# Kernel tuning notes

Hardware: AMD Instinct MI355X
Metric: run time of the kernel (lower is better)

The kernel has to match this reference:

```python
import jax, jax.numpy as jnp
import numpy as np

N_NODES = 50000
N_EDGES = 800000
N_GRAPHS = 64
IN_CH = 128
HID = [64, 128]
MLP_CH = [128, 64, 64, 64, 1]


def _glorot(key, fan_in, fan_out):
    lim = jnp.sqrt(6.0 / (fan_in + fan_out))
    return jax.random.uniform(key, (fan_in, fan_out), jnp.float32, -lim, lim)


def setup_inputs() -> dict:
    key = jax.random.key(0)
    ks = jax.random.split(key, 16)
    x = jax.random.normal(ks[0], (N_NODES, IN_CH), jnp.float32)
    edge_index = jax.random.randint(ks[1], (2, N_EDGES), 0, N_NODES, jnp.int64)
    batch = jnp.sort(jax.random.randint(ks[2], (N_NODES,), 0, N_GRAPHS, jnp.int64))
    inp = {"x": x, "edge_index": edge_index, "batch": batch}
    # GCNConv weights (x @ W + b)
    inp["W1"] = _glorot(ks[3], IN_CH, HID[0]);  inp["b1"] = jnp.zeros((HID[0],), jnp.float32)
    inp["W2"] = _glorot(ks[4], HID[0], HID[1]); inp["b2"] = jnp.zeros((HID[1],), jnp.float32)
    # MLP weights
    for i in range(4):
        inp[f"M{i+1}"] = _glorot(ks[5 + i], MLP_CH[i], MLP_CH[i + 1])
        inp[f"c{i+1}"] = jnp.zeros((MLP_CH[i + 1],), jnp.float32)
    return inp


def _gcn_conv(x, src, dst, dinv, W, b):
    # x' = D^-1/2 (A + I) D^-1/2 (x W) + b, via gather-scale-scatter over edges
    h = x @ W                                   # [N, F]
    norm = dinv[src] * dinv[dst]                # [E+N]
    msg = h[src] * norm[:, None]                # gather + scale
    out = jax.ops.segment_sum(msg, dst, num_segments=x.shape[0])
    return out + b


def reference(x, edge_index, batch, W1, b1, W2, b2, M1, c1, M2, c2, M3, c3, M4, c4):
    N = x.shape[0]
    x = x.astype(jnp.float32)
    # add self loops (PyG GCNConv default)
    loops = jnp.arange(N, dtype=edge_index.dtype)
    src = jnp.concatenate([edge_index[0], loops])
    dst = jnp.concatenate([edge_index[1], loops])
    deg = jax.ops.segment_sum(jnp.ones_like(src, jnp.float32), dst, num_segments=N)
    dinv = jnp.where(deg > 0, jax.lax.rsqrt(jnp.maximum(deg, 1.0)), 0.0)

    h = jax.nn.relu(_gcn_conv(x, src, dst, dinv, W1, b1))
    h = jax.nn.relu(_gcn_conv(h, src, dst, dinv, W2, b2))

    # global mean pool per graph
    sums = jax.ops.segment_sum(h, batch, num_segments=N_GRAPHS)
    cnts = jax.ops.segment_sum(jnp.ones((N,), jnp.float32), batch, num_segments=N_GRAPHS)
    g = sums / jnp.maximum(cnts, 1.0)[:, None]   # [G, 128]

    # MLP (eval mode: dropout is identity)
    g = jax.nn.leaky_relu(g @ M1 + c1, negative_slope=0.2)
    g = jax.nn.leaky_relu(g @ M2 + c2, negative_slope=0.1)
    g = jax.nn.leaky_relu(g @ M3 + c3, negative_slope=0.1)
    g = jax.nn.relu(g @ M4 + c4)
    return g
```

## Files before the change

### kernel.cpp

```cpp
#include <hip/hip_runtime.h>
#include <hip/hip_fp16.h>

#define N_NODES 50000
#define N_EDGES 800000
#define N_GRAPHS 64

#define SCAN_BLOCK 256
#define SCAN_ITEMS 4
#define SCAN_CHUNK (SCAN_BLOCK * SCAN_ITEMS)
#define NB_SCAN ((N_NODES + SCAN_CHUNK - 1) / SCAN_CHUNK)

#define FILL_STRIPES 256

struct __align__(8) h4v { __half2 a, b; };


__global__ void k_zero(int* __restrict__ deg, float* __restrict__ sums) {
    int i = blockIdx.x * 256 + threadIdx.x;
    if (i < N_NODES) deg[i] = 0;
    if (i < N_GRAPHS * 128) sums[i] = 0.f;
}


__global__ void k_deg_part(const int* __restrict__ dst, int* __restrict__ deg, int E) {
    const int range = blockIdx.x & 7;
    const int stripe = blockIdx.x >> 3;
    const int lo = range * (N_NODES / 8);
    const int hi = lo + (N_NODES / 8);
    for (int e = stripe * 256 + threadIdx.x; e < E; e += FILL_STRIPES * 256) {
        int d = dst[e];
        if (d >= lo && d < hi) atomicAdd(&deg[d], 1);
    }
}

__global__ void k_scan1(const int* __restrict__ deg, int* __restrict__ part) {
    __shared__ int lds[SCAN_BLOCK];
    int b = blockIdx.x, t = threadIdx.x;
    int base = b * SCAN_CHUNK + t * SCAN_ITEMS;
    int s = 0;
#pragma unroll
    for (int k = 0; k < SCAN_ITEMS; ++k) {
        int i = base + k;
        if (i < N_NODES) s += deg[i];
    }
    lds[t] = s;
    __syncthreads();
    for (int off = SCAN_BLOCK / 2; off > 0; off >>= 1) {
        if (t < off) lds[t] += lds[t + off];
        __syncthreads();
    }
    if (t == 0) part[b] = lds[0];
}

__global__ void k_scan3(const int* __restrict__ deg, const int* __restrict__ part,
                        int* __restrict__ row_ptr, int* __restrict__ fill,
                        float* __restrict__ dinv) {
    __shared__ int lds[SCAN_BLOCK];
    __shared__ int pl[64];
    __shared__ int basePfx;
    int b = blockIdx.x, t = threadIdx.x;
    if (t < NB_SCAN) pl[t] = part[t];
    int base = b * SCAN_CHUNK + t * SCAN_ITEMS;
    int v[SCAN_ITEMS];
    int s = 0;
#pragma unroll
    for (int k = 0; k < SCAN_ITEMS; ++k) {
        int i = base + k;
        v[k] = (i < N_NODES) ? deg[i] : 0;
        s += v[k];
    }
    lds[t] = s;
    __syncthreads();
    if (t == 0) {
        int acc = 0;
        for (int i = 0; i < b; ++i) acc += pl[i];
        basePfx = acc;
    }
    for (int off = 1; off < SCAN_BLOCK; off <<= 1) {
        int val = (t >= off) ? lds[t - off] : 0;
        __syncthreads();
        lds[t] += val;
        __syncthreads();
    }
    int excl = (t == 0 ? 0 : lds[t - 1]) + basePfx;
#pragma unroll
    for (int k = 0; k < SCAN_ITEMS; ++k) {
        int i = base + k;
        if (i < N_NODES) {
            row_ptr[i] = excl;
            fill[i] = excl;
            dinv[i] = rsqrtf((float)(v[k] + 1));
            excl += v[k];
            if (i == N_NODES - 1) row_ptr[N_NODES] = excl;
        }
    }
}

__global__ void k_fill_part(const int* __restrict__ src, const int* __restrict__ dst,
                            int* __restrict__ fill, unsigned short* __restrict__ csr, int E) {
    const int range = blockIdx.x & 7;
    const int stripe = blockIdx.x >> 3;
    const int lo = range * (N_NODES / 8);
    const int hi = lo + (N_NODES / 8);
    for (int e = stripe * 256 + threadIdx.x; e < E; e += FILL_STRIPES * 256) {
        int d = dst[e];
        if (d >= lo && d < hi) {
            int pos = atomicAdd(&fill[d], 1);
            csr[pos] = (unsigned short)src[e];
        }
    }
}


__global__ __launch_bounds__(256) void k_gemm1(const float* __restrict__ A,
                                               const float* __restrict__ W,
                                               const float* __restrict__ dscale,
                                               __half* __restrict__ Cout, int N) {
    const int FIN = 128;
    __shared__ __align__(16) float As[64 * (FIN + 2)];
    __shared__ __align__(16) float Wsm[FIN * 64];
    const int t = threadIdx.x;
    const int row0 = blockIdx.x * 64;

    const int NF4 = 64 * FIN / 4;
    for (int idx = t; idx < NF4; idx += 256) {
        int r = idx / (FIN / 4);
        int c4 = idx % (FIN / 4);
        float4 v = make_float4(0.f, 0.f, 0.f, 0.f);
        if (row0 + r < N) v = ((const float4*)(A + (size_t)(row0 + r) * FIN))[c4];
        float* p = &As[r * (FIN + 2) + c4 * 4];
        ((float2*)p)[0] = make_float2(v.x, v.y);
        ((float2*)p)[1] = make_float2(v.z, v.w);
    }
    for (int idx = t; idx < FIN * 16; idx += 256) {
        int r = idx / 16, c4 = idx % 16;
        *((float4*)&Wsm[r * 64 + c4 * 4]) = ((const float4*)(W + (size_t)r * 64))[c4];
    }
    __syncthreads();

    const int tc = (t & 15) * 4;
    const int tr = (t >> 4) * 4;
    float acc[4][4] = {};
#pragma unroll 4
    for (int k = 0; k < FIN; k += 2) {
        float2 a[4];
#pragma unroll
        for (int r = 0; r < 4; ++r)
            a[r] = *(const float2*)&As[(tr + r) * (FIN + 2) + k];
        float4 w0 = *(const float4*)&Wsm[k * 64 + tc];
        float4 w1 = *(const float4*)&Wsm[(k + 1) * 64 + tc];
#pragma unroll
        for (int r = 0; r < 4; ++r) {
            acc[r][0] = fmaf(a[r].x, w0.x, acc[r][0]);
            acc[r][1] = fmaf(a[r].x, w0.y, acc[r][1]);
            acc[r][2] = fmaf(a[r].x, w0.z, acc[r][2]);
            acc[r][3] = fmaf(a[r].x, w0.w, acc[r][3]);
            acc[r][0] = fmaf(a[r].y, w1.x, acc[r][0]);
            acc[r][1] = fmaf(a[r].y, w1.y, acc[r][1]);
            acc[r][2] = fmaf(a[r].y, w1.z, acc[r][2]);
            acc[r][3] = fmaf(a[r].y, w1.w, acc[r][3]);
        }
    }

#pragma unroll
    for (int r = 0; r < 4; ++r) {
        int row = row0 + tr + r;
        if (row < N) {
            float s = dscale[row];
            __half2* dsth = (__half2*)(Cout + (size_t)row * 64 + tc);
            dsth[0] = __floats2half2_rn(acc[r][0] * s, acc[r][1] * s);
            dsth[1] = __floats2half2_rn(acc[r][2] * s, acc[r][3] * s);
        }
    }
}


template <bool RELU>
__global__ void k_agg(const h4v* __restrict__ h, const float* __restrict__ dinv,
                      const int* __restrict__ row_ptr, const unsigned short* __restrict__ csr,
                      const float* __restrict__ bias, h4v* __restrict__ out, int N) {
    int node = blockIdx.x * 16 + (threadIdx.x >> 4);
    int lane = threadIdx.x & 15;
    if (node >= N) return;
    float di = dinv[node];
    h4v sv = h[(size_t)node * 16 + lane];
    float2 pa = __half22float2(sv.a), pb = __half22float2(sv.b);
    float x0 = pa.x, y0 = pa.y, z0 = pb.x, w0 = pb.y;
    float x1 = 0, y1 = 0, z1 = 0, w1 = 0;
    float x2 = 0, y2 = 0, z2 = 0, w2 = 0;
    float x3 = 0, y3 = 0, z3 = 0, w3 = 0;
    int beg = row_ptr[node], end = row_ptr[node + 1];
    int j = beg;
    for (; j + 4 <= end; j += 4) {
        int s0 = csr[j], s1 = csr[j + 1], s2 = csr[j + 2], s3 = csr[j + 3];
        h4v v0 = h[(size_t)s0 * 16 + lane];
        h4v v1 = h[(size_t)s1 * 16 + lane];
        h4v v2 = h[(size_t)s2 * 16 + lane];
        h4v v3 = h[(size_t)s3 * 16 + lane];
        float2 a0 = __half22float2(v0.a), b0 = __half22float2(v0.b);
        float2 a1 = __half22float2(v1.a), b1 = __half22float2(v1.b);
        float2 a2 = __half22float2(v2.a), b2 = __half22float2(v2.b);
        float2 a3 = __half22float2(v3.a), b3 = __half22float2(v3.b);
        x0 += a0.x; y0 += a0.y; z0 += b0.x; w0 += b0.y;
        x1 += a1.x; y1 += a1.y; z1 += b1.x; w1 += b1.y;
        x2 += a2.x; y2 += a2.y; z2 += b2.x; w2 += b2.y;
        x3 += a3.x; y3 += a3.y; z3 += b3.x; w3 += b3.y;
    }
    for (; j < end; ++j) {
        h4v v = h[(size_t)csr[j] * 16 + lane];
        float2 a = __half22float2(v.a), b = __half22float2(v.b);
        x0 += a.x; y0 += a.y; z0 += b.x; w0 += b.y;
    }
    float sx = (x0 + x1) + (x2 + x3);
    float sy = (y0 + y1) + (y2 + y3);
    float sz = (z0 + z1) + (z2 + z3);
    float sw = (w0 + w1) + (w2 + w3);
    h4v o;
    if (RELU) {
        float4 bv = ((const float4*)bias)[lane];
        float vx = fmaf(sx, di, bv.x); vx = vx > 0.f ? vx : 0.f;
        float vy = fmaf(sy, di, bv.y); vy = vy > 0.f ? vy : 0.f;
        float vz = fmaf(sz, di, bv.z); vz = vz > 0.f ? vz : 0.f;
        float vw = fmaf(sw, di, bv.w); vw = vw > 0.f ? vw : 0.f;
        o.a = __floats2half2_rn(di * vx, di * vy);
        o.b = __floats2half2_rn(di * vz, di * vw);
    } else {
        o.a = __floats2half2_rn(sx * di, sy * di);
        o.b = __floats2half2_rn(sz * di, sw * di);
    }
    out[(size_t)node * 16 + lane] = o;
}


__global__ __launch_bounds__(256) void k_gemm_pool(const __half2* __restrict__ A2,
                                                   const float* __restrict__ W,
                                                   const float* __restrict__ bias,
                                                   const int* __restrict__ batch,
                                                   float* __restrict__ sums, int N) {
    __shared__ __align__(16) float As[64 * 66];
    __shared__ __align__(16) float Wsm[64 * 64];
    __shared__ float red[16][68];
    __shared__ int batchLDS[64];
    const int t = threadIdx.x;
    const int row0 = blockIdx.x * 64;
    const int coff = blockIdx.y * 64;

    for (int idx = t; idx < 64 * 32; idx += 256) {
        int r = idx >> 5, c2 = idx & 31;
        float2 v = make_float2(0.f, 0.f);
        if (row0 + r < N) v = __half22float2(A2[(size_t)(row0 + r) * 32 + c2]);
        *(float2*)&As[r * 66 + c2 * 2] = v;
    }
    for (int idx = t; idx < 64 * 16; idx += 256) {
        int r = idx >> 4, c4 = idx & 15;
        *(float4*)&Wsm[r * 64 + c4 * 4] = *(const float4*)&W[(size_t)r * 128 + coff + c4 * 4];
    }
    if (t < 64) batchLDS[t] = batch[min(row0 + t, N - 1)];
    __syncthreads();

    const int tc = (t & 15) * 4;
    const int tr = (t >> 4) * 4;
    float acc[4][4] = {};
#pragma unroll 4
    for (int k = 0; k < 64; k += 2) {
        float2 a[4];
#pragma unroll
        for (int r = 0; r < 4; ++r)
            a[r] = *(const float2*)&As[(tr + r) * 66 + k];
        float4 w0 = *(const float4*)&Wsm[k * 64 + tc];
        float4 w1 = *(const float4*)&Wsm[(k + 1) * 64 + tc];
#pragma unroll
        for (int r = 0; r < 4; ++r) {
            acc[r][0] = fmaf(a[r].x, w0.x, acc[r][0]);
            acc[r][1] = fmaf(a[r].x, w0.y, acc[r][1]);
            acc[r][2] = fmaf(a[r].x, w0.z, acc[r][2]);
            acc[r][3] = fmaf(a[r].x, w0.w, acc[r][3]);
            acc[r][0] = fmaf(a[r].y, w1.x, acc[r][0]);
            acc[r][1] = fmaf(a[r].y, w1.y, acc[r][1]);
            acc[r][2] = fmaf(a[r].y, w1.z, acc[r][2]);
            acc[r][3] = fmaf(a[r].y, w1.w, acc[r][3]);
        }
    }

    float4 bv = *(const float4*)&bias[coff + tc];
    float v[4][4];
#pragma unroll
    for (int r = 0; r < 4; ++r) {
        bool valid = (row0 + tr + r) < N;
        v[r][0] = valid ? fmaxf(acc[r][0] + bv.x, 0.f) : 0.f;
        v[r][1] = valid ? fmaxf(acc[r][1] + bv.y, 0.f) : 0.f;
        v[r][2] = valid ? fmaxf(acc[r][2] + bv.z, 0.f) : 0.f;
        v[r][3] = valid ? fmaxf(acc[r][3] + bv.w, 0.f) : 0.f;
    }

    const int g0 = batchLDS[0], g1 = batchLDS[63];
    const int trg = t >> 4;
    for (int g = g0; g <= g1; ++g) {
        float p0 = 0.f, p1 = 0.f, p2 = 0.f, p3 = 0.f;
#pragma unroll
        for (int r = 0; r < 4; ++r) {
            if (batchLDS[tr + r] == g) { p0 += v[r][0]; p1 += v[r][1]; p2 += v[r][2]; p3 += v[r][3]; }
        }
        red[trg][tc + 0] = p0; red[trg][tc + 1] = p1;
        red[trg][tc + 2] = p2; red[trg][tc + 3] = p3;
        __syncthreads();
        for (int off = 8; off > 0; off >>= 1) {
            if (trg < off) {
#pragma unroll
                for (int c = 0; c < 4; ++c) red[trg][tc + c] += red[trg + off][tc + c];
            }
            __syncthreads();
        }
        if (t < 16) {
#pragma unroll
            for (int c = 0; c < 4; ++c)
                atomicAdd(&sums[g * 128 + coff + t * 4 + c], red[0][t * 4 + c]);
        }
        __syncthreads();
    }
}


__global__ void k_mlp(const float* __restrict__ sums, const int* __restrict__ batch, int N,
                      const float* __restrict__ M1, const float* __restrict__ c1,
                      const float* __restrict__ M2, const float* __restrict__ c2,
                      const float* __restrict__ M3, const float* __restrict__ c3,
                      const float* __restrict__ M4, const float* __restrict__ c4,
                      float* __restrict__ out) {
    __shared__ float g[128], t1[64], t2[64], t3[64];
    __shared__ float cntb;
    int b = blockIdx.x;
    int t = threadIdx.x;
    if (t == 0) {
        int lo = 0, hi = N;
        while (lo < hi) { int m = (lo + hi) >> 1; if (batch[m] < b) lo = m + 1; else hi = m; }
        int lb = lo;
        lo = 0; hi = N;
        while (lo < hi) { int m = (lo + hi) >> 1; if (batch[m] <= b) lo = m + 1; else hi = m; }
        cntb = fmaxf((float)(lo - lb), 1.0f);
    }
    __syncthreads();
    if (t < 128) g[t] = sums[b * 128 + t] / cntb;
    __syncthreads();
    if (t < 64) {
        float acc = c1[t];
        for (int k = 0; k < 128; ++k) acc = fmaf(g[k], M1[k * 64 + t], acc);
        t1[t] = acc >= 0.f ? acc : 0.2f * acc;
    }
    __syncthreads();
    if (t < 64) {
        float acc = c2[t];
        for (int k = 0; k < 64; ++k) acc = fmaf(t1[k], M2[k * 64 + t], acc);
        t2[t] = acc >= 0.f ? acc : 0.1f * acc;
    }
    __syncthreads();
    if (t < 64) {
        float acc = c3[t];
        for (int k = 0; k < 64; ++k) acc = fmaf(t2[k], M3[k * 64 + t], acc);
        t3[t] = acc >= 0.f ? acc : 0.1f * acc;
    }
    __syncthreads();
    if (t == 0) {
        float acc = c4[0];
        for (int k = 0; k < 64; ++k) acc = fmaf(t3[k], M4[k], acc);
        out[b] = fmaxf(acc, 0.f);
    }
}


extern "C" void kernel_launch(void* const* d_in, const int* in_sizes, int n_in,
                              void* d_out, int out_size, void* d_ws, size_t ws_size,
                              hipStream_t stream) {
    const float* x   = (const float*)d_in[0];
    const int*   ei  = (const int*)d_in[1];
    const int*   bat = (const int*)d_in[2];
    const float* W1  = (const float*)d_in[3];
    const float* b1  = (const float*)d_in[4];
    const float* W2  = (const float*)d_in[5];
    const float* b2  = (const float*)d_in[6];
    const float* M1  = (const float*)d_in[7];
    const float* c1  = (const float*)d_in[8];
    const float* M2  = (const float*)d_in[9];
    const float* c2  = (const float*)d_in[10];
    const float* M3  = (const float*)d_in[11];
    const float* c3  = (const float*)d_in[12];
    const float* M4  = (const float*)d_in[13];
    const float* c4  = (const float*)d_in[14];
    float* out = (float*)d_out;

    const int* src = ei;
    const int* dst = ei + N_EDGES;

    float* bufA    = (float*)d_ws;
    float* bufB    = bufA + (size_t)N_NODES * 64;
    float* dinv    = bufB + (size_t)N_NODES * 64;
    float* sums    = dinv + N_NODES;
    int*   deg     = (int*)(sums + N_GRAPHS * 128);
    int*   row_ptr = deg + N_NODES;
    int*   fill    = row_ptr + N_NODES + 1;
    int*   part    = fill + N_NODES;
    unsigned short* csr = (unsigned short*)(part + 64);

    k_zero<<<(N_NODES + 255) / 256, 256, 0, stream>>>(deg, sums);
    k_deg_part<<<8 * FILL_STRIPES, 256, 0, stream>>>(dst, deg, N_EDGES);
    k_scan1<<<NB_SCAN, SCAN_BLOCK, 0, stream>>>(deg, part);
    k_scan3<<<NB_SCAN, SCAN_BLOCK, 0, stream>>>(deg, part, row_ptr, fill, dinv);
    k_fill_part<<<8 * FILL_STRIPES, 256, 0, stream>>>(src, dst, fill, csr, N_EDGES);

    const int NBLK = (N_NODES + 63) / 64;
    const int ABLK = (N_NODES + 15) / 16;

    k_gemm1<<<NBLK, 256, 0, stream>>>(x, W1, dinv, (__half*)bufA, N_NODES);
    k_agg<true><<<ABLK, 256, 0, stream>>>(
        (const h4v*)bufA, dinv, row_ptr, csr, b1, (h4v*)bufB, N_NODES);

    k_agg<false><<<ABLK, 256, 0, stream>>>(
        (const h4v*)bufB, dinv, row_ptr, csr, nullptr, (h4v*)bufA, N_NODES);
    k_gemm_pool<<<dim3(NBLK, 2), 256, 0, stream>>>(
        (const __half2*)bufA, W2, b2, bat, sums, N_NODES);

    k_mlp<<<N_GRAPHS, 128, 0, stream>>>(sums, bat, N_NODES,
                                        M1, c1, M2, c2, M3, c3, M4, c4, out);
}
```

Baseline: 262.8 us.

## Split fp16 feature matrix into two 32-column planes for cache-friendly aggregation

```diff
diff --git a/kernel.cpp b/kernel.cpp
--- a/kernel.cpp
+++ b/kernel.cpp
@@ -162,12 +162,14 @@
         }
     }
 
+    const int plane = tc >> 5;
+    const int col = tc & 31;
 #pragma unroll
     for (int r = 0; r < 4; ++r) {
         int row = row0 + tr + r;
         if (row < N) {
             float s = dscale[row];
-            __half2* dsth = (__half2*)(Cout + (size_t)row * 64 + tc);
+            __half2* dsth = (__half2*)(Cout + (size_t)plane * N * 32 + (size_t)row * 32 + col);
             dsth[0] = __floats2half2_rn(acc[r][0] * s, acc[r][1] * s);
             dsth[1] = __floats2half2_rn(acc[r][2] * s, acc[r][3] * s);
         }
@@ -176,14 +178,14 @@
 
 
 template <bool RELU>
-__global__ void k_agg(const h4v* __restrict__ h, const float* __restrict__ dinv,
-                      const int* __restrict__ row_ptr, const unsigned short* __restrict__ csr,
-                      const float* __restrict__ bias, h4v* __restrict__ out, int N) {
-    int node = blockIdx.x * 16 + (threadIdx.x >> 4);
-    int lane = threadIdx.x & 15;
+__global__ void k_agg_half(const h4v* __restrict__ hplane, const float* __restrict__ dinv,
+                           const int* __restrict__ row_ptr, const unsigned short* __restrict__ csr,
+                           const float* __restrict__ biasHalf, h4v* __restrict__ outPlane, int N) {
+    int node = blockIdx.x * 32 + (threadIdx.x >> 3);
+    int lane = threadIdx.x & 7;
     if (node >= N) return;
     float di = dinv[node];
-    h4v sv = h[(size_t)node * 16 + lane];
+    h4v sv = hplane[(size_t)node * 8 + lane];
     float2 pa = __half22float2(sv.a), pb = __half22float2(sv.b);
     float x0 = pa.x, y0 = pa.y, z0 = pb.x, w0 = pb.y;
     float x1 = 0, y1 = 0, z1 = 0, w1 = 0;
@@ -193,10 +195,10 @@
     int j = beg;
     for (; j + 4 <= end; j += 4) {
         int s0 = csr[j], s1 = csr[j + 1], s2 = csr[j + 2], s3 = csr[j + 3];
-        h4v v0 = h[(size_t)s0 * 16 + lane];
-        h4v v1 = h[(size_t)s1 * 16 + lane];
-        h4v v2 = h[(size_t)s2 * 16 + lane];
-        h4v v3 = h[(size_t)s3 * 16 + lane];
+        h4v v0 = hplane[(size_t)s0 * 8 + lane];
+        h4v v1 = hplane[(size_t)s1 * 8 + lane];
+        h4v v2 = hplane[(size_t)s2 * 8 + lane];
+        h4v v3 = hplane[(size_t)s3 * 8 + lane];
         float2 a0 = __half22float2(v0.a), b0 = __half22float2(v0.b);
         float2 a1 = __half22float2(v1.a), b1 = __half22float2(v1.b);
         float2 a2 = __half22float2(v2.a), b2 = __half22float2(v2.b);
@@ -207,7 +209,7 @@
         x3 += a3.x; y3 += a3.y; z3 += b3.x; w3 += b3.y;
     }
     for (; j < end; ++j) {
-        h4v v = h[(size_t)csr[j] * 16 + lane];
+        h4v v = hplane[(size_t)csr[j] * 8 + lane];
         float2 a = __half22float2(v.a), b = __half22float2(v.b);
         x0 += a.x; y0 += a.y; z0 += b.x; w0 += b.y;
     }
@@ -217,7 +219,7 @@
     float sw = (w0 + w1) + (w2 + w3);
     h4v o;
     if (RELU) {
-        float4 bv = ((const float4*)bias)[lane];
+        float4 bv = ((const float4*)biasHalf)[lane];
         float vx = fmaf(sx, di, bv.x); vx = vx > 0.f ? vx : 0.f;
         float vy = fmaf(sy, di, bv.y); vy = vy > 0.f ? vy : 0.f;
         float vz = fmaf(sz, di, bv.z); vz = vz > 0.f ? vz : 0.f;
@@ -228,7 +230,7 @@
         o.a = __floats2half2_rn(sx * di, sy * di);
         o.b = __floats2half2_rn(sz * di, sw * di);
     }
-    out[(size_t)node * 16 + lane] = o;
+    outPlane[(size_t)node * 8 + lane] = o;
 }
 
 
@@ -247,8 +249,10 @@
 
     for (int idx = t; idx < 64 * 32; idx += 256) {
         int r = idx >> 5, c2 = idx & 31;
+        int plane = c2 >> 4, cc = c2 & 15;
         float2 v = make_float2(0.f, 0.f);
-        if (row0 + r < N) v = __half22float2(A2[(size_t)(row0 + r) * 32 + c2]);
+        if (row0 + r < N)
+            v = __half22float2(A2[(size_t)plane * N * 16 + (size_t)(row0 + r) * 16 + cc]);
         *(float2*)&As[r * 66 + c2 * 2] = v;
     }
     for (int idx = t; idx < 64 * 16; idx += 256) {
@@ -408,14 +412,19 @@
     k_fill_part<<<8 * FILL_STRIPES, 256, 0, stream>>>(src, dst, fill, csr, N_EDGES);
 
     const int NBLK = (N_NODES + 63) / 64;
-    const int ABLK = (N_NODES + 15) / 16;
+    const int HBLK = (N_NODES + 31) / 32;
+    const size_t PLANE = (size_t)N_NODES * 8;
 
     k_gemm1<<<NBLK, 256, 0, stream>>>(x, W1, dinv, (__half*)bufA, N_NODES);
-    k_agg<true><<<ABLK, 256, 0, stream>>>(
+    k_agg_half<true><<<HBLK, 256, 0, stream>>>(
         (const h4v*)bufA, dinv, row_ptr, csr, b1, (h4v*)bufB, N_NODES);
-
-    k_agg<false><<<ABLK, 256, 0, stream>>>(
+    k_agg_half<true><<<HBLK, 256, 0, stream>>>(
+        (const h4v*)bufA + PLANE, dinv, row_ptr, csr, b1 + 32, (h4v*)bufB + PLANE, N_NODES);
+
+    k_agg_half<false><<<HBLK, 256, 0, stream>>>(
         (const h4v*)bufB, dinv, row_ptr, csr, nullptr, (h4v*)bufA, N_NODES);
+    k_agg_half<false><<<HBLK, 256, 0, stream>>>(
+        (const h4v*)bufB + PLANE, dinv, row_ptr, csr, nullptr, (h4v*)bufA + PLANE, N_NODES);
     k_gemm_pool<<<dim3(NBLK, 2), 256, 0, stream>>>(
         (const __half2*)bufA, W2, b2, bat, sums, N_NODES);
 
```

Result: slower. 270.4 us (+2.9%).
